# Optimization experiments

Measured on AMD Instinct MI355X. Metric: run time of the kernel, lower is better.

Reference implementation:

```python
import jax, jax.numpy as jnp
import numpy as np

NUM_HEADS = 8
TOP_K = 32
LN_EPS = 1e-5
RENORM_EPS = 1e-5


def _split_heads(x):
    # [B, S, D] -> [B, H, S, d]
    B, S, D = x.shape
    return x.reshape(B, S, NUM_HEADS, D // NUM_HEADS).transpose(0, 2, 1, 3)


def setup_inputs() -> dict:
    key = jax.random.key(0)
    k1, k2, k3, k4 = jax.random.split(key, 4)
    B, S, D, H = 2, 2048, 1024, NUM_HEADS
    q = jax.random.normal(k1, (B, S, D), dtype=jnp.float32)
    k = jax.random.normal(k2, (B, S, D), dtype=jnp.float32)
    v = jax.random.normal(k3, (B, S, D), dtype=jnp.float32)
    attention_weight = jax.random.normal(k4, (B, H, S, S), dtype=jnp.float32)
    gamma = jnp.ones((D,), dtype=jnp.float32)
    beta = jnp.zeros((D,), dtype=jnp.float32)
    return {"q": q, "k": k, "v": v, "attention_weight": attention_weight,
            "gamma": gamma, "beta": beta}


def reference(q, k, v, attention_weight, gamma, beta):
    B, S, D = q.shape
    qh = _split_heads(q)  # [B,H,S,d]
    kh = _split_heads(k)
    vh = _split_heads(v)
    # Unscaled QK^T (faithful to source: no /sqrt(d))
    scores = jnp.einsum("bhqd,bhkd->bhqk", qh, kh)
    probs = jax.nn.softmax(scores, axis=-1)
    # top-k mask via double argsort: rank of each key by descending weight
    rank = jnp.argsort(jnp.argsort(-attention_weight, axis=-1), axis=-1)
    top_mask = (rank < TOP_K).astype(probs.dtype)
    probs = probs * top_mask
    probs = probs / (jnp.sum(probs, axis=-1, keepdims=True) + RENORM_EPS)
    out = jnp.einsum("bhqk,bhkd->bhqd", probs, vh)
    out = out.transpose(0, 2, 1, 3).reshape(B, S, D)
    # LayerNorm over last dim
    mu = jnp.mean(out, axis=-1, keepdims=True)
    var = jnp.var(out, axis=-1, keepdims=True)
    out = (out - mu) * jax.lax.rsqrt(var + LN_EPS) * gamma + beta
    return out
```

## Files before the change

### kernel.cpp

```cpp
#include <hip/hip_runtime.h>
#include <hip/hip_bf16.h>
#include <stdint.h>

#define BB 2
#define SS 2048
#define DD 1024
#define HH 8
#define HD 128
#define TOPK 32
#define ROWS (BB*HH*SS)

__global__ __launch_bounds__(256) void topk_kernel(const float* __restrict__ aw,
                                                   int* __restrict__ idx_out) {
    const int row = blockIdx.x;
    const float* p = aw + (size_t)row * SS;
    const int t = threadIdx.x;
    float4 v0 = *(const float4*)(p + 4 * t);
    float4 v1 = *(const float4*)(p + 1024 + 4 * t);
    float vals[8] = {v0.x, v0.y, v0.z, v0.w, v1.x, v1.y, v1.z, v1.w};
    unsigned long long key[8];
#pragma unroll
    for (int i = 0; i < 8; i++) {
        int e = (i < 4) ? (4 * t + i) : (1024 + 4 * t + (i - 4));
        unsigned u = __float_as_uint(vals[i]);
        unsigned sk = (u & 0x80000000u) ? ~u : (u | 0x80000000u);
        key[i] = ((unsigned long long)sk << 11) | (unsigned)(2047 - e);
    }
    __shared__ int s_cnt;
    __shared__ int s_red[4];
    __shared__ unsigned long long s_cand[256];
    const int lane = t & 63, wv = t >> 6;

    unsigned thr0 = __float_as_uint(1.76f) | 0x80000000u;
    unsigned long long T = ((unsigned long long)thr0 << 11) | 2047ull;

    if (t == 0) s_cnt = 0;
    __syncthreads();
#pragma unroll
    for (int i = 0; i < 8; i++) {
        if (key[i] > T) {
            int pos = atomicAdd(&s_cnt, 1);
            if (pos < 256) s_cand[pos] = key[i];
        }
    }
    __syncthreads();

    if (s_cnt < TOPK || s_cnt > 256) {
        unsigned long long lo = 0, hi = ~0ull;
        if (s_cnt > 256) lo = T; else hi = T;
        T = lo + ((hi - lo) >> 1);
        for (int it = 0; it < 40; ++it) {
            int c = 0;
#pragma unroll
            for (int i = 0; i < 8; i++) c += (key[i] > T) ? 1 : 0;
            for (int off = 32; off; off >>= 1) c += __shfl_down(c, off, 64);
            if (lane == 0) s_red[wv] = c;
            __syncthreads();
            int tot = s_red[0] + s_red[1] + s_red[2] + s_red[3];
            if (tot >= TOPK && tot <= 256) break;
            if (tot > 256) lo = T; else hi = T;
            T = lo + ((hi - lo) >> 1);
            __syncthreads();
        }
        if (t == 0) s_cnt = 0;
        __syncthreads();
#pragma unroll
        for (int i = 0; i < 8; i++) {
            if (key[i] > T) {
                int pos = atomicAdd(&s_cnt, 1);
                if (pos < 256) s_cand[pos] = key[i];
            }
        }
        __syncthreads();
    }

    const int C = s_cnt < 256 ? s_cnt : 256;
    if (t < C) {
        unsigned long long mk = s_cand[t];
        int rank = 0;
        for (int j = 0; j < C; ++j)
            rank += (s_cand[j] > mk) ? 1 : 0;
        if (rank < TOPK)
            idx_out[(size_t)row * TOPK + rank] = 2047 - (int)(mk & 2047ull);
    }
}

typedef float f32x4 __attribute__((ext_vector_type(4)));
typedef _Float16 f16x8 __attribute__((ext_vector_type(8)));
typedef _Float16 f16x4 __attribute__((ext_vector_type(4)));

#define KPAD 136

__global__ __launch_bounds__(256) void stats_kernel(const float* __restrict__ q,
                                                    const float* __restrict__ k,
                                                    float* __restrict__ ws_m,
                                                    float* __restrict__ ws_l) {
    __shared__ __align__(16) _Float16 Qs[128 * KPAD];
    __shared__ __align__(16) _Float16 Ks[128 * KPAD];
    const int blk = blockIdx.x & 255;
    const int half = blockIdx.x >> 8;
    const int bh = blk >> 4;
    const int qt = blk & 15;
    const int b = bh >> 3, h = bh & 7;
    const int t = threadIdx.x;
    const int wv = t >> 6, lane = t & 63;
    const int l16 = lane & 15, quad = lane >> 4;

    const float* qbase = q + ((size_t)(b * SS + qt * 128) * DD + h * HD);
#pragma unroll
    for (int i = 0; i < 16; ++i) {
        int fi = t + 256 * i;
        int r = fi >> 5, c4 = fi & 31;
        float4 f = *(const float4*)(qbase + (size_t)r * DD + c4 * 4);
        *(f16x4*)&Qs[r * KPAD + c4 * 4] =
            (f16x4){(_Float16)f.x, (_Float16)f.y, (_Float16)f.z, (_Float16)f.w};
    }
    float mrun[2][4], lrun[2][4];
#pragma unroll
    for (int a = 0; a < 2; a++)
#pragma unroll
        for (int r2 = 0; r2 < 4; r2++) { mrun[a][r2] = -INFINITY; lrun[a][r2] = 0.f; }

    const float* kbase = k + ((size_t)(b * SS) * DD + h * HD);
    for (int kt = half * 8; kt < half * 8 + 8; ++kt) {
        __syncthreads();
#pragma unroll
        for (int i = 0; i < 16; ++i) {
            int fi = t + 256 * i;
            int r = fi >> 5, c4 = fi & 31;
            float4 f = *(const float4*)(kbase + (size_t)(kt * 128 + r) * DD + c4 * 4);
            *(f16x4*)&Ks[r * KPAD + c4 * 4] =
                (f16x4){(_Float16)f.x, (_Float16)f.y, (_Float16)f.z, (_Float16)f.w};
        }
        __syncthreads();
        f32x4 acc[2][8];
#pragma unroll
        for (int a = 0; a < 2; a++)
#pragma unroll
            for (int n = 0; n < 8; n++) acc[a][n] = (f32x4){0.f, 0.f, 0.f, 0.f};
#pragma unroll
        for (int ks = 0; ks < 4; ++ks) {
            f16x8 af[2], bfr[8];
#pragma unroll
            for (int a = 0; a < 2; a++)
                af[a] = *(const f16x8*)&Qs[(wv * 32 + a * 16 + l16) * KPAD + ks * 32 + quad * 8];
#pragma unroll
            for (int n = 0; n < 8; n++)
                bfr[n] = *(const f16x8*)&Ks[(n * 16 + l16) * KPAD + ks * 32 + quad * 8];
#pragma unroll
            for (int a = 0; a < 2; a++)
#pragma unroll
                for (int n = 0; n < 8; n++)
                    acc[a][n] = __builtin_amdgcn_mfma_f32_16x16x32_f16(af[a], bfr[n], acc[a][n], 0, 0, 0);
        }
#pragma unroll
        for (int a = 0; a < 2; a++) {
#pragma unroll
            for (int r2 = 0; r2 < 4; r2++) {
                float tm = acc[a][0][r2];
#pragma unroll
                for (int n = 1; n < 8; n++) tm = fmaxf(tm, acc[a][n][r2]);
#pragma unroll
                for (int off = 1; off < 16; off <<= 1) tm = fmaxf(tm, __shfl_xor(tm, off, 64));
                float tl = 0.f;
#pragma unroll
                for (int n = 0; n < 8; n++) tl += __expf(acc[a][n][r2] - tm);
#pragma unroll
                for (int off = 1; off < 16; off <<= 1) tl += __shfl_xor(tl, off, 64);
                float mo = mrun[a][r2];
                float mn = fmaxf(mo, tm);
                lrun[a][r2] = lrun[a][r2] * __expf(mo - mn) + tl * __expf(tm - mn);
                mrun[a][r2] = mn;
            }
        }
    }
    if (l16 == 0) {
#pragma unroll
        for (int a = 0; a < 2; a++)
#pragma unroll
            for (int r2 = 0; r2 < 4; r2++) {
                int rrow = qt * 128 + wv * 32 + a * 16 + quad * 4 + r2;
                size_t g = (size_t)half * ROWS + (size_t)bh * SS + rrow;
                ws_m[g] = mrun[a][r2];
                ws_l[g] = lrun[a][r2];
            }
    }
}

__global__ __launch_bounds__(128) void attnout_kernel(const float* __restrict__ q,
                                                      const float* __restrict__ k,
                                                      const float* __restrict__ v,
                                                      const int* __restrict__ idx_ws,
                                                      const float* __restrict__ ws_m,
                                                      const float* __restrict__ ws_l,
                                                      float* __restrict__ out) {
    const int bh = blockIdx.x & 15;
    const int s = blockIdx.x >> 4;
    const int R = (bh << 11) | s;
    const int b = bh >> 3, h = bh & 7;
    const int t = threadIdx.x;
    __shared__ float q_l[128];
    __shared__ int idx_l[32];
    __shared__ float e_l[32];
    __shared__ float w_l[32];
    const float* qrow = q + ((size_t)(b * SS + s) * DD + h * HD);
    q_l[t] = qrow[t];
    if (t < 32) idx_l[t] = idx_ws[(size_t)R * TOPK + t];
    __syncthreads();
    const float m0 = ws_m[R], m1 = ws_m[(size_t)ROWS + R];
    const float l0 = ws_l[R], l1 = ws_l[(size_t)ROWS + R];
    const float m = fmaxf(m0, m1);
    const float Z = l0 * __expf(m0 - m) + l1 * __expf(m1 - m);
    const int l32 = t & 31, g = t >> 5;
    float4 q4 = *(const float4*)&q_l[l32 * 4];
    const float* kb = k + ((size_t)b * SS * DD + h * HD);
#pragma unroll
    for (int p = 0; p < 8; ++p) {
        int i = p * 4 + g;
        int ki = idx_l[i];
        float4 kv = *(const float4*)(kb + (size_t)ki * DD + l32 * 4);
        float d = q4.x * kv.x + q4.y * kv.y + q4.z * kv.z + q4.w * kv.w;
#pragma unroll
        for (int off = 1; off < 32; off <<= 1) d += __shfl_xor(d, off, 64);
        if (l32 == 0) e_l[i] = __expf(d - m);
    }
    __syncthreads();
    if (t < 32) {
        float e = e_l[t];
        float ssum = e;
#pragma unroll
        for (int off = 1; off < 32; off <<= 1) ssum += __shfl_xor(ssum, off, 64);
        float den = ssum + 1e-5f * Z;
        w_l[t] = e / den;
    }
    __syncthreads();
    const float* vb = v + ((size_t)b * SS * DD + h * HD);
    float accv = 0.f;
#pragma unroll 8
    for (int i = 0; i < 32; ++i) {
        accv += w_l[i] * vb[(size_t)idx_l[i] * DD + t];
    }
    out[((size_t)(b * SS + s) * DD) + h * HD + t] = accv;
}

__global__ __launch_bounds__(256) void ln_kernel(float* __restrict__ out,
                                                 const float* __restrict__ gamma,
                                                 const float* __restrict__ beta) {
    const int row = blockIdx.x;
    float* p = out + (size_t)row * DD;
    const int t = threadIdx.x;
    float x[4];
#pragma unroll
    for (int i = 0; i < 4; i++) x[i] = p[t + 256 * i];
    float sum = x[0] + x[1] + x[2] + x[3];
    __shared__ float red[4];
    const int lane = t & 63, wv = t >> 6;
    for (int off = 32; off; off >>= 1) sum += __shfl_down(sum, off, 64);
    if (lane == 0) red[wv] = sum;
    __syncthreads();
    float mean = (red[0] + red[1] + red[2] + red[3]) * (1.f / DD);
    __syncthreads();
    float vs = 0.f;
#pragma unroll
    for (int i = 0; i < 4; i++) { float d = x[i] - mean; vs += d * d; }
    for (int off = 32; off; off >>= 1) vs += __shfl_down(vs, off, 64);
    if (lane == 0) red[wv] = vs;
    __syncthreads();
    float var = (red[0] + red[1] + red[2] + red[3]) * (1.f / DD);
    float inv = rsqrtf(var + 1e-5f);
#pragma unroll
    for (int i = 0; i < 4; i++) {
        int c = t + 256 * i;
        p[c] = (x[i] - mean) * inv * gamma[c] + beta[c];
    }
}

extern "C" void kernel_launch(void* const* d_in, const int* in_sizes, int n_in,
                              void* d_out, int out_size, void* d_ws, size_t ws_size,
                              hipStream_t stream) {
    const float* q = (const float*)d_in[0];
    const float* k = (const float*)d_in[1];
    const float* v = (const float*)d_in[2];
    const float* aw = (const float*)d_in[3];
    const float* gamma = (const float*)d_in[4];
    const float* beta = (const float*)d_in[5];
    float* out = (float*)d_out;

    int* idx_ws = (int*)d_ws;
    float* ws_m = (float*)((char*)d_ws + (size_t)ROWS * TOPK * sizeof(int));
    float* ws_l = ws_m + 2 * ROWS;

    hipLaunchKernelGGL(topk_kernel, dim3(ROWS), dim3(256), 0, stream, aw, idx_ws);
    hipLaunchKernelGGL(stats_kernel, dim3(512), dim3(256), 0, stream, q, k, ws_m, ws_l);
    hipLaunchKernelGGL(attnout_kernel, dim3(ROWS), dim3(128), 0, stream, q, k, v, idx_ws, ws_m, ws_l, out);
    hipLaunchKernelGGL(ln_kernel, dim3(BB * SS), dim3(256), 0, stream, out, gamma, beta);
}
```

Before: 530.5 us.

## Pre-convert K to fp16 head layout, split stats 4-way, warp-per-row attnout

Adds a kernel that converts K once to fp16 in a head-major layout, so the stats kernel loads fp16 tiles instead of reconverting fp32 K for every query tile. Q fragments now stay in registers rather than shared memory. The key dimension is split four ways instead of two, doubling the block count. The attention-output kernel now handles one query row per wavefront using shuffles instead of shared memory and block barriers. The cost is an extra launch, extra workspace, and a four-way merge of the partial statistics.

```diff
diff --git a/kernel.cpp b/kernel.cpp
--- a/kernel.cpp
+++ b/kernel.cpp
@@ -9,6 +9,11 @@
 #define HD 128
 #define TOPK 32
 #define ROWS (BB*HH*SS)
+#define SPLITK 4
+
+typedef float f32x4 __attribute__((ext_vector_type(4)));
+typedef _Float16 f16x8 __attribute__((ext_vector_type(8)));
+typedef _Float16 f16x4 __attribute__((ext_vector_type(4)));
 
 __global__ __launch_bounds__(256) void topk_kernel(const float* __restrict__ aw,
                                                    int* __restrict__ idx_out) {
@@ -85,52 +90,61 @@
     }
 }
 
-typedef float f32x4 __attribute__((ext_vector_type(4)));
-typedef _Float16 f16x8 __attribute__((ext_vector_type(8)));
-typedef _Float16 f16x4 __attribute__((ext_vector_type(4)));
+__global__ __launch_bounds__(256) void convk_kernel(const float* __restrict__ k,
+                                                    _Float16* __restrict__ kh) {
+    const int f = blockIdx.x * 256 + threadIdx.x;
+    const int row = f >> 8;
+    const int c4 = f & 255;
+    const int h = c4 >> 5, d4 = c4 & 31;
+    const int b = row >> 11, s = row & 2047;
+    float4 kv = ((const float4*)k)[f];
+    f16x4 o = {(_Float16)kv.x, (_Float16)kv.y, (_Float16)kv.z, (_Float16)kv.w};
+    *(f16x4*)&kh[(((size_t)(b * HH + h) * SS + s) * HD) + d4 * 4] = o;
+}
 
 #define KPAD 136
 
 __global__ __launch_bounds__(256) void stats_kernel(const float* __restrict__ q,
-                                                    const float* __restrict__ k,
+                                                    const _Float16* __restrict__ kh,
                                                     float* __restrict__ ws_m,
                                                     float* __restrict__ ws_l) {
-    __shared__ __align__(16) _Float16 Qs[128 * KPAD];
     __shared__ __align__(16) _Float16 Ks[128 * KPAD];
-    const int blk = blockIdx.x & 255;
-    const int half = blockIdx.x >> 8;
-    const int bh = blk >> 4;
-    const int qt = blk & 15;
+    const int bh = blockIdx.x & 15;
+    const int qt = (blockIdx.x >> 4) & 15;
+    const int quarter = blockIdx.x >> 8;
     const int b = bh >> 3, h = bh & 7;
     const int t = threadIdx.x;
     const int wv = t >> 6, lane = t & 63;
     const int l16 = lane & 15, quad = lane >> 4;
 
-    const float* qbase = q + ((size_t)(b * SS + qt * 128) * DD + h * HD);
-#pragma unroll
-    for (int i = 0; i < 16; ++i) {
-        int fi = t + 256 * i;
-        int r = fi >> 5, c4 = fi & 31;
-        float4 f = *(const float4*)(qbase + (size_t)r * DD + c4 * 4);
-        *(f16x4*)&Qs[r * KPAD + c4 * 4] =
-            (f16x4){(_Float16)f.x, (_Float16)f.y, (_Float16)f.z, (_Float16)f.w};
-    }
+    const float* qb = q + ((size_t)(b * SS + qt * 128)) * DD + h * HD;
+    f16x8 qfrag[2][4];
+#pragma unroll
+    for (int a = 0; a < 2; a++)
+#pragma unroll
+        for (int ks = 0; ks < 4; ks++) {
+            const float* src = qb + (size_t)(wv * 32 + a * 16 + l16) * DD + ks * 32 + quad * 8;
+            float4 x0 = *(const float4*)src;
+            float4 x1 = *(const float4*)(src + 4);
+            qfrag[a][ks] = (f16x8){(_Float16)x0.x, (_Float16)x0.y, (_Float16)x0.z, (_Float16)x0.w,
+                                   (_Float16)x1.x, (_Float16)x1.y, (_Float16)x1.z, (_Float16)x1.w};
+        }
+
     float mrun[2][4], lrun[2][4];
 #pragma unroll
     for (int a = 0; a < 2; a++)
 #pragma unroll
         for (int r2 = 0; r2 < 4; r2++) { mrun[a][r2] = -INFINITY; lrun[a][r2] = 0.f; }
 
-    const float* kbase = k + ((size_t)(b * SS) * DD + h * HD);
-    for (int kt = half * 8; kt < half * 8 + 8; ++kt) {
+    const _Float16* khb = kh + (size_t)bh * SS * HD;
+    for (int kt = quarter * 4; kt < quarter * 4 + 4; ++kt) {
         __syncthreads();
 #pragma unroll
-        for (int i = 0; i < 16; ++i) {
-            int fi = t + 256 * i;
-            int r = fi >> 5, c4 = fi & 31;
-            float4 f = *(const float4*)(kbase + (size_t)(kt * 128 + r) * DD + c4 * 4);
-            *(f16x4*)&Ks[r * KPAD + c4 * 4] =
-                (f16x4){(_Float16)f.x, (_Float16)f.y, (_Float16)f.z, (_Float16)f.w};
+        for (int j = 0; j < 8; ++j) {
+            int c = t + 256 * j;
+            int r = c >> 4, c16 = c & 15;
+            f16x8 val = *(const f16x8*)&khb[(size_t)(kt * 128 + r) * HD + c16 * 8];
+            *(f16x8*)&Ks[r * KPAD + c16 * 8] = val;
         }
         __syncthreads();
         f32x4 acc[2][8];
@@ -140,10 +154,7 @@
             for (int n = 0; n < 8; n++) acc[a][n] = (f32x4){0.f, 0.f, 0.f, 0.f};
 #pragma unroll
         for (int ks = 0; ks < 4; ++ks) {
-            f16x8 af[2], bfr[8];
-#pragma unroll
-            for (int a = 0; a < 2; a++)
-                af[a] = *(const f16x8*)&Qs[(wv * 32 + a * 16 + l16) * KPAD + ks * 32 + quad * 8];
+            f16x8 bfr[8];
 #pragma unroll
             for (int n = 0; n < 8; n++)
                 bfr[n] = *(const f16x8*)&Ks[(n * 16 + l16) * KPAD + ks * 32 + quad * 8];
@@ -151,7 +162,7 @@
             for (int a = 0; a < 2; a++)
 #pragma unroll
                 for (int n = 0; n < 8; n++)
-                    acc[a][n] = __builtin_amdgcn_mfma_f32_16x16x32_f16(af[a], bfr[n], acc[a][n], 0, 0, 0);
+                    acc[a][n] = __builtin_amdgcn_mfma_f32_16x16x32_f16(qfrag[a][ks], bfr[n], acc[a][n], 0, 0, 0);
         }
 #pragma unroll
         for (int a = 0; a < 2; a++) {
@@ -180,14 +191,14 @@
 #pragma unroll
             for (int r2 = 0; r2 < 4; r2++) {
                 int rrow = qt * 128 + wv * 32 + a * 16 + quad * 4 + r2;
-                size_t g = (size_t)half * ROWS + (size_t)bh * SS + rrow;
+                size_t g = (size_t)quarter * ROWS + (size_t)bh * SS + rrow;
                 ws_m[g] = mrun[a][r2];
                 ws_l[g] = lrun[a][r2];
             }
     }
 }
 
-__global__ __launch_bounds__(128) void attnout_kernel(const float* __restrict__ q,
+__global__ __launch_bounds__(256) void attnout_kernel(const float* __restrict__ q,
                                                       const float* __restrict__ k,
                                                       const float* __restrict__ v,
                                                       const int* __restrict__ idx_ws,
@@ -195,52 +206,50 @@
                                                       const float* __restrict__ ws_l,
                                                       float* __restrict__ out) {
     const int bh = blockIdx.x & 15;
-    const int s = blockIdx.x >> 4;
+    const int sg = blockIdx.x >> 4;
+    const int wv = threadIdx.x >> 6, lane = threadIdx.x & 63;
+    const int s = sg * 4 + wv;
+    const int b = bh >> 3, h = bh & 7;
     const int R = (bh << 11) | s;
-    const int b = bh >> 3, h = bh & 7;
-    const int t = threadIdx.x;
-    __shared__ float q_l[128];
-    __shared__ int idx_l[32];
-    __shared__ float e_l[32];
-    __shared__ float w_l[32];
-    const float* qrow = q + ((size_t)(b * SS + s) * DD + h * HD);
-    q_l[t] = qrow[t];
-    if (t < 32) idx_l[t] = idx_ws[(size_t)R * TOPK + t];
-    __syncthreads();
-    const float m0 = ws_m[R], m1 = ws_m[(size_t)ROWS + R];
-    const float l0 = ws_l[R], l1 = ws_l[(size_t)ROWS + R];
-    const float m = fmaxf(m0, m1);
-    const float Z = l0 * __expf(m0 - m) + l1 * __expf(m1 - m);
-    const int l32 = t & 31, g = t >> 5;
-    float4 q4 = *(const float4*)&q_l[l32 * 4];
-    const float* kb = k + ((size_t)b * SS * DD + h * HD);
-#pragma unroll
-    for (int p = 0; p < 8; ++p) {
-        int i = p * 4 + g;
-        int ki = idx_l[i];
-        float4 kv = *(const float4*)(kb + (size_t)ki * DD + l32 * 4);
-        float d = q4.x * kv.x + q4.y * kv.y + q4.z * kv.z + q4.w * kv.w;
-#pragma unroll
-        for (int off = 1; off < 32; off <<= 1) d += __shfl_xor(d, off, 64);
-        if (l32 == 0) e_l[i] = __expf(d - m);
-    }
-    __syncthreads();
-    if (t < 32) {
-        float e = e_l[t];
-        float ssum = e;
-#pragma unroll
-        for (int off = 1; off < 32; off <<= 1) ssum += __shfl_xor(ssum, off, 64);
-        float den = ssum + 1e-5f * Z;
-        w_l[t] = e / den;
-    }
-    __syncthreads();
-    const float* vb = v + ((size_t)b * SS * DD + h * HD);
-    float accv = 0.f;
-#pragma unroll 8
-    for (int i = 0; i < 32; ++i) {
-        accv += w_l[i] * vb[(size_t)idx_l[i] * DD + t];
-    }
-    out[((size_t)(b * SS + s) * DD) + h * HD + t] = accv;
+
+    int idxr = idx_ws[(size_t)R * TOPK + (lane & 31)];
+
+    float mp0 = ws_m[R], mp1 = ws_m[(size_t)ROWS + R];
+    float mp2 = ws_m[2 * (size_t)ROWS + R], mp3 = ws_m[3 * (size_t)ROWS + R];
+    float m = fmaxf(fmaxf(mp0, mp1), fmaxf(mp2, mp3));
+    float Z = ws_l[R] * __expf(mp0 - m) + ws_l[(size_t)ROWS + R] * __expf(mp1 - m)
+            + ws_l[2 * (size_t)ROWS + R] * __expf(mp2 - m)
+            + ws_l[3 * (size_t)ROWS + R] * __expf(mp3 - m);
+
+    const int sel = lane >> 1, half = lane & 1;
+    const int ki = __shfl(idxr, sel);
+    const float4* qr = (const float4*)(q + ((size_t)(b * SS) + s) * DD + h * HD + half * 64);
+    const float4* kr = (const float4*)(k + ((size_t)(b * SS) + ki) * DD + h * HD + half * 64);
+    float d = 0.f;
+#pragma unroll
+    for (int c = 0; c < 16; ++c) {
+        float4 a = qr[c], kk = kr[c];
+        d += a.x * kk.x + a.y * kk.y + a.z * kk.z + a.w * kk.w;
+    }
+    d += __shfl_xor(d, 1);
+    float e = __shfl(__expf(d - m), 2 * (lane & 31));
+    float Ssum = e;
+#pragma unroll
+    for (int off = 1; off < 32; off <<= 1) Ssum += __shfl_xor(Ssum, off);
+    float w = e / (Ssum + 1e-5f * Z);
+
+    const float* vbh = v + (size_t)b * SS * DD + h * HD;
+    float a0 = 0.f, a1 = 0.f;
+#pragma unroll
+    for (int i = 0; i < TOPK; ++i) {
+        int vi = __shfl(idxr, i);
+        float wi = __shfl(w, i);
+        float2 vv = *(const float2*)(vbh + (size_t)vi * DD + 2 * lane);
+        a0 += wi * vv.x;
+        a1 += wi * vv.y;
+    }
+    float* orow = out + ((size_t)(b * SS) + s) * DD + h * HD;
+    ((float2*)orow)[lane] = make_float2(a0, a1);
 }
 
 __global__ __launch_bounds__(256) void ln_kernel(float* __restrict__ out,
@@ -262,7 +271,7 @@
     __syncthreads();
     float vs = 0.f;
 #pragma unroll
-    for (int i = 0; i < 4; i++) { float d = x[i] - mean; vs += d * d; }
+    for (int i = 0; i < 4; i++) { float dd = x[i] - mean; vs += dd * dd; }
     for (int off = 32; off; off >>= 1) vs += __shfl_down(vs, off, 64);
     if (lane == 0) red[wv] = vs;
     __syncthreads();
@@ -286,12 +295,15 @@
     const float* beta = (const float*)d_in[5];
     float* out = (float*)d_out;
 
-    int* idx_ws = (int*)d_ws;
-    float* ws_m = (float*)((char*)d_ws + (size_t)ROWS * TOPK * sizeof(int));
-    float* ws_l = ws_m + 2 * ROWS;
+    char* wp = (char*)d_ws;
+    int* idx_ws = (int*)wp;                    wp += (size_t)ROWS * TOPK * sizeof(int);
+    float* ws_m = (float*)wp;                  wp += (size_t)SPLITK * ROWS * sizeof(float);
+    float* ws_l = (float*)wp;                  wp += (size_t)SPLITK * ROWS * sizeof(float);
+    _Float16* kh = (_Float16*)wp;
 
     hipLaunchKernelGGL(topk_kernel, dim3(ROWS), dim3(256), 0, stream, aw, idx_ws);
-    hipLaunchKernelGGL(stats_kernel, dim3(512), dim3(256), 0, stream, q, k, ws_m, ws_l);
-    hipLaunchKernelGGL(attnout_kernel, dim3(ROWS), dim3(128), 0, stream, q, k, v, idx_ws, ws_m, ws_l, out);
+    hipLaunchKernelGGL(convk_kernel, dim3(4096), dim3(256), 0, stream, k, kh);
+    hipLaunchKernelGGL(stats_kernel, dim3(256 * SPLITK), dim3(256), 0, stream, q, kh, ws_m, ws_l);
+    hipLaunchKernelGGL(attnout_kernel, dim3(8192), dim3(256), 0, stream, q, k, v, idx_ws, ws_m, ws_l, out);
     hipLaunchKernelGGL(ln_kernel, dim3(BB * SS), dim3(256), 0, stream, out, gamma, beta);
 }
```

After: 599.8 us. 1.13x slower.
